# Kernel tuning notes

Measured on AMD Instinct MI355X. Metric: run time of the kernel, lower is better.

The kernel has to match this reference:

```python
import math
import jax, jax.numpy as jnp
import numpy as np

K = 4          # beats_per_bar
POS_DIM = 32   # fourier pos-embed dim


def setup_inputs() -> dict:
    key = jax.random.key(0)
    k1, k2, k3 = jax.random.split(key, 3)
    B, M, D = 8, 8192, 1024
    beat_emb = jax.random.normal(k1, (B, M, D), dtype=jnp.float32)
    W = jax.random.normal(k2, (D, D + POS_DIM), dtype=jnp.float32) * 0.02  # nn.Linear weight [out, in]
    b = jax.random.normal(k3, (D,), dtype=jnp.float32) * 0.02
    return {"beat_emb": beat_emb, "W": W, "b": b}


def _fourier_features(pos, dim):
    # pos: [Mb] in [0,1] -> [Mb, dim] (dim even, so no zero-pad branch needed)
    half = dim // 2
    freqs = jnp.exp(jnp.linspace(0.0, math.log(1000.0), half)).astype(pos.dtype)
    ang = pos[:, None] * freqs  # [Mb, half]
    return jnp.concatenate([jnp.sin(ang), jnp.cos(ang)], axis=-1)


def reference(beat_emb, W, b):
    B, M, D = beat_emb.shape
    Mb = (M + K - 1) // K
    pad = Mb * K - M
    x = jnp.pad(beat_emb, ((0, 0), (0, pad), (0, 0))) if pad else beat_emb
    # fused segment mean: [B, Mb, K, D] -> sum -> divide by actual segment length
    sums = x.reshape(B, Mb, K, D).sum(axis=2)
    counts = jnp.minimum(K, M - jnp.arange(Mb) * K).astype(beat_emb.dtype)  # [Mb]
    out = sums / counts[None, :, None]  # [B, Mb, D]
    # fourier positional features on normalized bar index (same for every batch row)
    idx = jnp.arange(Mb, dtype=beat_emb.dtype)
    pos = jnp.clip(idx / max(1, Mb - 1), 0.0, 1.0)
    ff = _fourier_features(pos, POS_DIM)                     # [Mb, POS_DIM]
    ff = jnp.broadcast_to(ff[None], (B, Mb, POS_DIM))
    h = jnp.concatenate([out, ff], axis=-1)                  # [B, Mb, D+POS_DIM]
    return jnp.einsum('bmi,oi->bmo', h, W) + b               # Linear: x @ W.T + b
```

## Files before the change

kernel.cpp:

```cpp
#include <hip/hip_runtime.h>
#include <math.h>
#include <stdint.h>
#include <stddef.h>

typedef short bf16x8 __attribute__((ext_vector_type(8)));
typedef short bf16x4 __attribute__((ext_vector_type(4)));
typedef float f32x4  __attribute__((ext_vector_type(4)));

#define BATCH   8
#define D_IN    1024
#define POSD    32
#define KD      1056
#define KP      1088
#define MBARS   2048
#define MROWS   16384
#define NOUT    1024

__device__ __forceinline__ short f2bf(float f) {
    unsigned u = __builtin_bit_cast(unsigned, f);
    u += 0x7fffu + ((u >> 16) & 1u);
    return (short)(u >> 16);
}

__device__ __forceinline__ void async_load16(const short* g, short* l) {
    __builtin_amdgcn_global_load_lds((__attribute__((address_space(1))) void*)g,
                                     (__attribute__((address_space(3))) void*)l,
                                     16, 0, 0);
}

__global__ __launch_bounds__(256) void prep(const float* __restrict__ x,
                                            const float* __restrict__ W,
                                            short* __restrict__ h,
                                            short* __restrict__ Wb) {
    const int t = threadIdx.x;
    const int bid = blockIdx.x;
    if (bid < MROWS) {
        const float4* src = (const float4*)(x + (size_t)bid * 4096);
        float4 s0 = src[t], s1 = src[t + 256], s2 = src[t + 512], s3 = src[t + 768];
        bf16x4 o = { f2bf((s0.x + s1.x + s2.x + s3.x) * 0.25f),
                     f2bf((s0.y + s1.y + s2.y + s3.y) * 0.25f),
                     f2bf((s0.z + s1.z + s2.z + s3.z) * 0.25f),
                     f2bf((s0.w + s1.w + s2.w + s3.w) * 0.25f) };
        short* hr = h + (size_t)bid * KP;
        *(bf16x4*)(hr + t * 4) = o;
        if (t < POSD) {
            const int mb = bid & (MBARS - 1);
            float pos = (float)mb * (1.0f / (float)(MBARS - 1));
            float fr  = expf((float)(t & 15) * (6.907755278982137f / 15.0f));
            float ang = pos * fr;
            hr[D_IN + t] = f2bf((t < 16) ? sinf(ang) : cosf(ang));
            hr[KD + t]   = 0;
        }
    } else {
        const int r = bid - MROWS;
        const float* wr = W + (size_t)r * KD;
        short* br = Wb + (size_t)r * KP;
        float4 v = *(const float4*)(wr + t * 4);
        bf16x4 o = { f2bf(v.x), f2bf(v.y), f2bf(v.z), f2bf(v.w) };
        *(bf16x4*)(br + t * 4) = o;
        if (t < 8) {
            float4 u = *(const float4*)(wr + 1024 + t * 4);
            bf16x4 p = { f2bf(u.x), f2bf(u.y), f2bf(u.z), f2bf(u.w) };
            *(bf16x4*)(br + 1024 + t * 4) = p;
            *(bf16x4*)(br + KD + t * 4)   = (bf16x4){0, 0, 0, 0};
        }
    }
}

__global__ __launch_bounds__(256) void gemm_bt(const short* __restrict__ A,
                                               const short* __restrict__ B,
                                               const float* __restrict__ bias,
                                               float* __restrict__ C) {
    __shared__ short As[128 * 64];
    __shared__ short Bs[128 * 64];

    const int tid  = threadIdx.x;
    const int wave = tid >> 6;
    const int lane = tid & 63;
    const int wrow = wave >> 1;
    const int wcol = wave & 1;

    const int m0 = blockIdx.x * 128;
    const int n0 = blockIdx.y * 128;

    const int r8   = tid >> 3;
    const int soct = (tid & 7) ^ (r8 & 7);
    const short* ag = A + (size_t)(m0 + r8) * KP + soct * 8;
    const short* bg = B + (size_t)(n0 + r8) * KP + soct * 8;
    short* al = As + wave * 512;
    short* bl = Bs + wave * 512;

    const int r  = lane & 15;
    const int q  = lane >> 4;
    const int rx = r & 7;
    const short* afr = As + (wrow * 64 + r) * 64;
    const short* bfr = Bs + (wcol * 64 + r) * 64;
    const int sl0 = ((q    ) ^ rx) * 8;
    const int sl1 = ((4 + q) ^ rx) * 8;

    f32x4 acc[4][4] = {};

    for (int k0 = 0; k0 < KP; k0 += 64) {
        __syncthreads();
#pragma unroll
        for (int i = 0; i < 4; ++i) {
            async_load16(ag + k0 + (size_t)i * 32 * KP, al + i * 2048);
            async_load16(bg + k0 + (size_t)i * 32 * KP, bl + i * 2048);
        }
        __syncthreads();

#pragma unroll
        for (int s = 0; s < 2; ++s) {
            const int sl = s ? sl1 : sl0;
            bf16x8 a[4], b[4];
#pragma unroll
            for (int i = 0; i < 4; ++i) {
                a[i] = *(const bf16x8*)(afr + i * 1024 + sl);
                b[i] = *(const bf16x8*)(bfr + i * 1024 + sl);
            }
#pragma unroll
            for (int i = 0; i < 4; ++i)
#pragma unroll
                for (int j = 0; j < 4; ++j)
                    acc[i][j] = __builtin_amdgcn_mfma_f32_16x16x32_bf16(a[i], b[j], acc[i][j], 0, 0, 0);
        }
    }

    const int rr0 = m0 + wrow * 64 + (q << 2);
    const int c0  = n0 + wcol * 64 + r;
    float bv[4];
#pragma unroll
    for (int j = 0; j < 4; ++j) bv[j] = bias[c0 + j * 16];
#pragma unroll
    for (int i = 0; i < 4; ++i)
#pragma unroll
        for (int rg = 0; rg < 4; ++rg) {
            float* cp = C + (size_t)(rr0 + i * 16 + rg) * NOUT;
#pragma unroll
            for (int j = 0; j < 4; ++j)
                cp[c0 + j * 16] = acc[i][j][rg] + bv[j];
        }
}

extern "C" void kernel_launch(void* const* d_in, const int* in_sizes, int n_in,
                              void* d_out, int out_size, void* d_ws, size_t ws_size,
                              hipStream_t stream) {
    const float* x    = (const float*)d_in[0];
    const float* W    = (const float*)d_in[1];
    const float* bias = (const float*)d_in[2];
    float* out = (float*)d_out;

    short* Wb = (short*)d_ws;
    short* h  = (short*)((char*)d_ws + (size_t)NOUT * KP * sizeof(short));

    prep   <<<dim3(MROWS + NOUT), dim3(256), 0, stream>>>(x, W, h, Wb);
    gemm_bt<<<dim3(MROWS / 128, NOUT / 128), dim3(256), 0, stream>>>(h, Wb, bias, out);
}
```

Before: 423.1 us.

## Replace LDS-staged GEMM with register double-buffered direct global loads

The GEMM no longer stages tiles in shared memory. Each wave now loads its MFMA fragments straight from global memory into registers, double-buffered across k-steps, which removes the __syncthreads barriers and LDS traffic. The block index is also remapped so that consecutive blocks spread across M tiles for the same N, aiming at better L2 reuse. In exchange, the two column-waves in a block load the same A rows separately and the two row-waves load the same B rows, and the 16-byte-per-lane strided global loads depend on L2/cache bandwidth instead of the shared-memory staging.

```diff
diff --git a/kernel.cpp b/kernel.cpp
--- a/kernel.cpp
+++ b/kernel.cpp
@@ -20,12 +20,6 @@
     unsigned u = __builtin_bit_cast(unsigned, f);
     u += 0x7fffu + ((u >> 16) & 1u);
     return (short)(u >> 16);
-}
-
-__device__ __forceinline__ void async_load16(const short* g, short* l) {
-    __builtin_amdgcn_global_load_lds((__attribute__((address_space(1))) void*)g,
-                                     (__attribute__((address_space(3))) void*)l,
-                                     16, 0, 0);
 }
 
 __global__ __launch_bounds__(256) void prep(const float* __restrict__ x,
@@ -67,64 +61,75 @@
     }
 }
 
-__global__ __launch_bounds__(256) void gemm_bt(const short* __restrict__ A,
-                                               const short* __restrict__ B,
-                                               const float* __restrict__ bias,
-                                               float* __restrict__ C) {
-    __shared__ short As[128 * 64];
-    __shared__ short Bs[128 * 64];
-
+__global__ __launch_bounds__(256) void gemm_reg(const short* __restrict__ A,
+                                                const short* __restrict__ B,
+                                                const float* __restrict__ bias,
+                                                float* __restrict__ C) {
     const int tid  = threadIdx.x;
     const int wave = tid >> 6;
     const int lane = tid & 63;
     const int wrow = wave >> 1;
     const int wcol = wave & 1;
 
-    const int m0 = blockIdx.x * 128;
-    const int n0 = blockIdx.y * 128;
+    const int bid = blockIdx.x;
+    const int l   = bid >> 3;
+    const int mt  = (bid & 7) * 16 + (l >> 3);
+    const int nt  = l & 7;
+    const int m0  = mt * 128;
+    const int n0  = nt * 128;
 
-    const int r8   = tid >> 3;
-    const int soct = (tid & 7) ^ (r8 & 7);
-    const short* ag = A + (size_t)(m0 + r8) * KP + soct * 8;
-    const short* bg = B + (size_t)(n0 + r8) * KP + soct * 8;
-    short* al = As + wave * 512;
-    short* bl = Bs + wave * 512;
+    const int r = lane & 15;
+    const int q = lane >> 4;
 
-    const int r  = lane & 15;
-    const int q  = lane >> 4;
-    const int rx = r & 7;
-    const short* afr = As + (wrow * 64 + r) * 64;
-    const short* bfr = Bs + (wcol * 64 + r) * 64;
-    const int sl0 = ((q    ) ^ rx) * 8;
-    const int sl1 = ((4 + q) ^ rx) * 8;
+    const short* ap = A + (size_t)(m0 + wrow * 64 + r) * KP + q * 8;
+    const short* bp = B + (size_t)(n0 + wcol * 64 + r) * KP + q * 8;
 
     f32x4 acc[4][4] = {};
+    bf16x8 a0[4], b0[4], a1[4], b1[4];
 
-    for (int k0 = 0; k0 < KP; k0 += 64) {
-        __syncthreads();
+#pragma unroll
+    for (int i = 0; i < 4; ++i) {
+        a0[i] = *(const bf16x8*)(ap + (size_t)i * 16 * KP);
+        b0[i] = *(const bf16x8*)(bp + (size_t)i * 16 * KP);
+    }
+
+    for (int k0 = 0; k0 < KP - 64; k0 += 64) {
 #pragma unroll
         for (int i = 0; i < 4; ++i) {
-            async_load16(ag + k0 + (size_t)i * 32 * KP, al + i * 2048);
-            async_load16(bg + k0 + (size_t)i * 32 * KP, bl + i * 2048);
+            a1[i] = *(const bf16x8*)(ap + (size_t)i * 16 * KP + k0 + 32);
+            b1[i] = *(const bf16x8*)(bp + (size_t)i * 16 * KP + k0 + 32);
         }
-        __syncthreads();
-
 #pragma unroll
-        for (int s = 0; s < 2; ++s) {
-            const int sl = s ? sl1 : sl0;
-            bf16x8 a[4], b[4];
+        for (int i = 0; i < 4; ++i)
 #pragma unroll
-            for (int i = 0; i < 4; ++i) {
-                a[i] = *(const bf16x8*)(afr + i * 1024 + sl);
-                b[i] = *(const bf16x8*)(bfr + i * 1024 + sl);
-            }
+            for (int j = 0; j < 4; ++j)
+                acc[i][j] = __builtin_amdgcn_mfma_f32_16x16x32_bf16(a0[i], b0[j], acc[i][j], 0, 0, 0);
 #pragma unroll
-            for (int i = 0; i < 4; ++i)
+        for (int i = 0; i < 4; ++i) {
+            a0[i] = *(const bf16x8*)(ap + (size_t)i * 16 * KP + k0 + 64);
+            b0[i] = *(const bf16x8*)(bp + (size_t)i * 16 * KP + k0 + 64);
+        }
 #pragma unroll
-                for (int j = 0; j < 4; ++j)
-                    acc[i][j] = __builtin_amdgcn_mfma_f32_16x16x32_bf16(a[i], b[j], acc[i][j], 0, 0, 0);
-        }
+        for (int i = 0; i < 4; ++i)
+#pragma unroll
+            for (int j = 0; j < 4; ++j)
+                acc[i][j] = __builtin_amdgcn_mfma_f32_16x16x32_bf16(a1[i], b1[j], acc[i][j], 0, 0, 0);
     }
+#pragma unroll
+    for (int i = 0; i < 4; ++i) {
+        a1[i] = *(const bf16x8*)(ap + (size_t)i * 16 * KP + (KP - 32));
+        b1[i] = *(const bf16x8*)(bp + (size_t)i * 16 * KP + (KP - 32));
+    }
+#pragma unroll
+    for (int i = 0; i < 4; ++i)
+#pragma unroll
+        for (int j = 0; j < 4; ++j)
+            acc[i][j] = __builtin_amdgcn_mfma_f32_16x16x32_bf16(a0[i], b0[j], acc[i][j], 0, 0, 0);
+#pragma unroll
+    for (int i = 0; i < 4; ++i)
+#pragma unroll
+        for (int j = 0; j < 4; ++j)
+            acc[i][j] = __builtin_amdgcn_mfma_f32_16x16x32_bf16(a1[i], b1[j], acc[i][j], 0, 0, 0);
 
     const int rr0 = m0 + wrow * 64 + (q << 2);
     const int c0  = n0 + wcol * 64 + r;
@@ -153,6 +158,6 @@
     short* Wb = (short*)d_ws;
     short* h  = (short*)((char*)d_ws + (size_t)NOUT * KP * sizeof(short));
 
-    prep   <<<dim3(MROWS + NOUT), dim3(256), 0, stream>>>(x, W, h, Wb);
-    gemm_bt<<<dim3(MROWS / 128, NOUT / 128), dim3(256), 0, stream>>>(h, Wb, bias, out);
+    prep    <<<dim3(MROWS + NOUT), dim3(256), 0, stream>>>(x, W, h, Wb);
+    gemm_reg<<<dim3((MROWS / 128) * (NOUT / 128)), dim3(256), 0, stream>>>(h, Wb, bias, out);
 }
```

Result: slower. 506.7 us (+19.8%).
